# Optimization experiments

Hardware: AMD Instinct MI355X
Metric: run time of the kernel (lower is better)

The kernel has to match this reference:

```python
import jax, jax.numpy as jnp
import numpy as np

IN_FEATURES = 4096
OUT_FEATURES = 4096  # % 16 == 0, so pad_out = 0
BATCH, SEQ = 4, 2048


def setup_inputs() -> dict:
    key = jax.random.key(0)
    k_x, k_w, k_b = jax.random.split(key, 3)
    # int8 activations and weights (W8A8)
    x = jax.random.randint(k_x, (BATCH, SEQ, IN_FEATURES), -128, 128, dtype=jnp.int32).astype(jnp.int8)
    # weight stored as (in_features, out_features), matching qlinear.weight layout
    weight = jax.random.randint(k_w, (IN_FEATURES, OUT_FEATURES), -128, 128, dtype=jnp.int32).astype(jnp.int8)
    # a: scalar input scale; b: per-output-channel dequant/requant scale
    a = jnp.full((1, 1), 0.0123, dtype=jnp.float32)
    b = jax.random.uniform(k_b, (1, OUT_FEATURES), dtype=jnp.float32, minval=0.001, maxval=0.02)
    return {"x": x, "weight": weight, "a": a, "b": b}


def reference(x, weight, a, b):
    # x: [B, S, K] int8; weight: [K, N] int8; a: [1,1] f32; b: [1,N] f32
    x_shape = x.shape
    x2d = x.reshape(-1, x_shape[-1])
    acc = jnp.matmul(x2d, weight, preferred_element_type=jnp.int32)
    # fused dequant (scalar a) + per-channel requant (b), round-to-nearest, saturate to int8
    y_f = acc.astype(jnp.float32) * a * b  # [T, N]
    y = jnp.clip(jnp.round(y_f), -128.0, 127.0).astype(jnp.int8)
    return y.reshape(*x_shape[:-1], -1)
```

## Files before the change

kernel.cpp:

```cpp
#include <hip/hip_runtime.h>
#include <stdint.h>

#define M_DIM 8192
#define N_DIM 4096
#define K_DIM 4096
#define BM 128
#define BN 128
#define BK 64

typedef int v4i __attribute__((ext_vector_type(4)));
typedef unsigned u32;

__device__ __forceinline__ void gll16(const void* g, void* l) {
  __builtin_amdgcn_global_load_lds(
      (const __attribute__((address_space(1))) void*)g,
      (__attribute__((address_space(3))) void*)l, 16, 0, 0);
}

__device__ __forceinline__ u32 pack4(const int4 v) {
  return (v.x & 0xffu) | ((v.y & 0xffu) << 8) | ((v.z & 0xffu) << 16) |
         ((u32)(v.w & 0xffu) << 24);
}

__device__ __forceinline__ bool hdr_is_i32(const int* __restrict__ X, int tid,
                                           int* ok) {
  if (tid == 0) *ok = 1;
  __syncthreads();
  int good = 1;
  for (int i = tid; i < 1024; i += 256) {
    const int w = X[i];
    good &= (w == (int)(int8_t)(w & 0xff));
  }
  if (!good) atomicAnd(ok, 0);
  __syncthreads();
  return *ok != 0;
}

__global__ __launch_bounds__(256) void detect_i32(const int* __restrict__ X,
                                                  u32* __restrict__ flag) {
  __shared__ int ok;
  const bool i32 = hdr_is_i32(X, threadIdx.x, &ok);
  if (threadIdx.x == 0) *flag = i32 ? 1u : 0u;
}

__global__ __launch_bounds__(256) void pack_xw_f(const void* __restrict__ Xin,
                                                 const void* __restrict__ Wv,
                                                 u32* __restrict__ xout,
                                                 int8_t* __restrict__ WT) {
  __shared__ u32 lds[64 * 21];
  __shared__ int ok;
  const int tid = threadIdx.x;
  const bool i32 = hdr_is_i32((const int*)Xin, tid, &ok);

  if (blockIdx.x < 8192) {
    const int base = blockIdx.x * 1024 + tid;
    if (i32) {
      const int4* in = (const int4*)Xin;
#pragma unroll
      for (int j = 0; j < 4; ++j) {
        const int idx = base + j * 256;
        xout[idx] = pack4(in[idx]);
      }
    } else {
      const u32* in = (const u32*)Xin;
#pragma unroll
      for (int j = 0; j < 4; ++j) {
        const int idx = base + j * 256;
        xout[idx] = in[idx];
      }
    }
    return;
  }

  const int bid = blockIdx.x - 8192;
  const int tk = bid & 63;
  const int tn = bid >> 6;
  const int k0 = tk * 64, n0 = tn * 64;

#pragma unroll
  for (int j = 0; j < 4; ++j) {
    const int id = j * 256 + tid;
    const int k = id >> 4, c = id & 15;
    u32 word;
    if (i32) {
      const int4 v =
          *(const int4*)((const int*)Wv + (size_t)(k0 + k) * N_DIM + n0 + c * 4);
      word = pack4(v);
    } else {
      word = *(const u32*)((const int8_t*)Wv + (size_t)(k0 + k) * N_DIM + n0 +
                           c * 4);
    }
    lds[k * 21 + c] = word;
  }
  __syncthreads();
  const int kd = tid & 15, nq = tid >> 4;
  const u32 d0 = lds[(kd * 4 + 0) * 21 + nq];
  const u32 d1 = lds[(kd * 4 + 1) * 21 + nq];
  const u32 d2 = lds[(kd * 4 + 2) * 21 + nq];
  const u32 d3 = lds[(kd * 4 + 3) * 21 + nq];
  u32* outp = (u32*)WT;
#pragma unroll
  for (int i = 0; i < 4; ++i) {
    const u32 e = ((d0 >> (8 * i)) & 0xffu) | (((d1 >> (8 * i)) & 0xffu) << 8) |
                  (((d2 >> (8 * i)) & 0xffu) << 16) |
                  (((d3 >> (8 * i)) & 0xffu) << 24);
    const int n = n0 + nq * 4 + i;
    outp[(size_t)n * (K_DIM / 4) + (k0 / 4) + kd] = e;
  }
}

__global__ __launch_bounds__(256) void packT_w_f(const void* __restrict__ Wv,
                                                 int8_t* __restrict__ WT,
                                                 const int* __restrict__ Xhdr) {
  __shared__ u32 lds[64 * 21];
  __shared__ int ok;
  const int tid = threadIdx.x;
  const bool i32 = hdr_is_i32(Xhdr, tid, &ok);
  const int tk = blockIdx.x & 63;
  const int tn = blockIdx.x >> 6;
  const int k0 = tk * 64, n0 = tn * 64;

#pragma unroll
  for (int j = 0; j < 4; ++j) {
    const int id = j * 256 + tid;
    const int k = id >> 4, c = id & 15;
    u32 word;
    if (i32) {
      const int4 v =
          *(const int4*)((const int*)Wv + (size_t)(k0 + k) * N_DIM + n0 + c * 4);
      word = pack4(v);
    } else {
      word = *(const u32*)((const int8_t*)Wv + (size_t)(k0 + k) * N_DIM + n0 +
                           c * 4);
    }
    lds[k * 21 + c] = word;
  }
  __syncthreads();
  const int kd = tid & 15, nq = tid >> 4;
  const u32 d0 = lds[(kd * 4 + 0) * 21 + nq];
  const u32 d1 = lds[(kd * 4 + 1) * 21 + nq];
  const u32 d2 = lds[(kd * 4 + 2) * 21 + nq];
  const u32 d3 = lds[(kd * 4 + 3) * 21 + nq];
  u32* outp = (u32*)WT;
#pragma unroll
  for (int i = 0; i < 4; ++i) {
    const u32 e = ((d0 >> (8 * i)) & 0xffu) | (((d1 >> (8 * i)) & 0xffu) << 8) |
                  (((d2 >> (8 * i)) & 0xffu) << 16) |
                  (((d3 >> (8 * i)) & 0xffu) << 24);
    const int n = n0 + nq * 4 + i;
    outp[(size_t)n * (K_DIM / 4) + (k0 / 4) + kd] = e;
  }
}

__device__ __forceinline__ void epilogue(const v4i acc[4][4], float a,
                                         const float* __restrict__ bScale,
                                         int* __restrict__ Y, int bm, int bn,
                                         int wm, int wn, int quad, int l16) {
  const int nBase = bn * BN + wn * 64 + l16;
  float bs[4];
#pragma unroll
  for (int ni = 0; ni < 4; ++ni) bs[ni] = bScale[nBase + ni * 16];
#pragma unroll
  for (int mi = 0; mi < 4; ++mi) {
    const int m0 = bm * BM + wm * 64 + mi * 16 + quad * 4;
#pragma unroll
    for (int r = 0; r < 4; ++r) {
      int* row = Y + (size_t)(m0 + r) * N_DIM + nBase;
#pragma unroll
      for (int ni = 0; ni < 4; ++ni) {
        float v = ((float)acc[mi][ni][r] * a) * bs[ni];
        v = rintf(v);
        v = fminf(fmaxf(v, -128.f), 127.f);
        row[ni * 16] = (int)v;
      }
    }
  }
}

__device__ __forceinline__ void rd4(v4i* f, const int8_t* base, int off) {
#pragma unroll
  for (int i = 0; i < 4; ++i) f[i] = *(const v4i*)(base + off + i * 1024);
}

__device__ __forceinline__ void mfma16(v4i acc[8][4], int row, const v4i* a,
                                       const v4i* b) {
#pragma unroll
  for (int mi = 0; mi < 4; ++mi)
#pragma unroll
    for (int ni = 0; ni < 4; ++ni)
      acc[row + mi][ni] = __builtin_amdgcn_mfma_i32_16x16x64_i8(
          a[mi], b[ni], acc[row + mi][ni], 0, 0, 0);
}

__device__ __forceinline__ void compute64(const int8_t* aBase,
                                          const int8_t* bBase, int soff,
                                          v4i acc[8][4]) {
  v4i bf[4], af[4], ag[4];
  rd4(bf, bBase, soff);
  rd4(af, aBase, soff);
  __builtin_amdgcn_s_setprio(1);
  mfma16(acc, 0, af, bf);
  rd4(ag, aBase, soff + 4096);
  mfma16(acc, 4, ag, bf);
  __builtin_amdgcn_s_setprio(0);
}

__global__ __launch_bounds__(512, 2) void gemm_256(
    const int8_t* __restrict__ X, const int8_t* __restrict__ WT,
    const float* __restrict__ aScale, const float* __restrict__ bScale,
    int* __restrict__ Y) {
  __shared__ __align__(16) int8_t lds[131072];
  const int tid = threadIdx.x;
  const int lane = tid & 63;
  const int wave = tid >> 6;
  const int quad = lane >> 4, l16 = lane & 15;
  const int wm = wave >> 2, wn = wave & 3;

  const int swzb = (blockIdx.x & 7) * 64 + (blockIdx.x >> 3);
  const int bn = swzb & 15, bm = swzb >> 4;

  const int clog = (((tid & 3) ^ ((tid >> 3) & 3)) << 4);
  const int pc = quad ^ ((l16 >> 1) & 3);

  const int8_t* xa = X + (size_t)(bm * 256 + (tid >> 2)) * K_DIM + clog;
  const int8_t* xb = WT + (size_t)(bn * 256 + (tid >> 2)) * K_DIM + clog;
  int8_t* ldsA = lds + tid * 16;
  int8_t* ldsB = lds + 65536 + tid * 16;
  const int8_t* aBase = lds + (wm * 128 + l16) * 64 + pc * 16;
  const int8_t* bBase = lds + 65536 + (wn * 64 + l16) * 64 + pc * 16;

  v4i acc[8][4] = {};

#pragma unroll
  for (int t = 0; t < 2; ++t) {
    gll16(xa + t * 64, ldsA + t * 16384);
    gll16(xa + (size_t)128 * K_DIM + t * 64, ldsA + t * 16384 + 8192);
    gll16(xb + t * 64, ldsB + t * 16384);
    gll16(xb + (size_t)128 * K_DIM + t * 64, ldsB + t * 16384 + 8192);
  }
  asm volatile("s_waitcnt vmcnt(0)" ::: "memory");
  __builtin_amdgcn_s_barrier();

  for (int G = 0; G < 32; ++G) {
    const int g0 = 2 * G;
    if (G < 31) {
#pragma unroll
      for (int t = 2; t < 4; ++t) {
        const int poff = ((g0 + t) & 3) << 14;
        const int8_t* sa = xa + (size_t)(g0 + t) * 64;
        const int8_t* sb = xb + (size_t)(g0 + t) * 64;
        gll16(sa, ldsA + poff);
        gll16(sa + (size_t)128 * K_DIM, ldsA + poff + 8192);
        gll16(sb, ldsB + poff);
        gll16(sb + (size_t)128 * K_DIM, ldsB + poff + 8192);
      }
    }
    compute64(aBase, bBase, (g0 & 3) << 14, acc);
    compute64(aBase, bBase, ((g0 + 1) & 3) << 14, acc);
    asm volatile("s_waitcnt vmcnt(0)" ::: "memory");
    __builtin_amdgcn_s_barrier();
  }

  const float a = aScale[0];
  const int nBase = bn * 256 + wn * 64 + l16;
  float bs[4];
#pragma unroll
  for (int ni = 0; ni < 4; ++ni) bs[ni] = bScale[nBase + ni * 16];
#pragma unroll
  for (int mi = 0; mi < 8; ++mi) {
    const int m0 = bm * 256 + wm * 128 + mi * 16 + quad * 4;
#pragma unroll
    for (int r = 0; r < 4; ++r) {
      int* row = Y + (size_t)(m0 + r) * N_DIM + nBase;
#pragma unroll
      for (int ni = 0; ni < 4; ++ni) {
        float v = ((float)acc[mi][ni][r] * a) * bs[ni];
        v = rintf(v);
        v = fminf(fmaxf(v, -128.f), 127.f);
        row[ni * 16] = (int)v;
      }
    }
  }
}

__global__ __launch_bounds__(256) void gemm_inA(
    const void* __restrict__ Xv, const int8_t* __restrict__ WT,
    const float* __restrict__ aScale, const float* __restrict__ bScale,
    int* __restrict__ Y, const u32* __restrict__ flag) {
  __shared__ __align__(16) int8_t As[BM * BK];
  __shared__ __align__(16) int8_t Bs[BN * BK];
  const bool i32 = (*flag != 0);
  const int tid = threadIdx.x;
  const int lane = tid & 63, wave = tid >> 6;
  const int quad = lane >> 4, l16 = lane & 15;
  const int wm = wave & 1, wn = wave >> 1;
  const int bn = blockIdx.x & 31;
  const int bm = blockIdx.x >> 5;

  const int r0 = tid >> 2;
  const int c0 = (tid & 3) * 16;
  const int8_t* Bg0 = WT + (size_t)(bn * BN + r0) * K_DIM + c0;
  const int8_t* Bg1 = Bg0 + (size_t)64 * K_DIM;
  int8_t* Al0 = As + tid * 16;
  int8_t* Al1 = Al0 + 4096;
  int8_t* Bl0 = Bs + tid * 16;
  int8_t* Bl1 = Bl0 + 4096;

  v4i acc[4][4] = {};
  const int8_t* aLds = As + (wm * 64 + l16) * BK + quad * 16;
  const int8_t* bLds = Bs + (wn * 64 + l16) * BK + quad * 16;

  if (i32) {
    const int* Xg0 = (const int*)Xv + (size_t)(bm * BM + r0) * K_DIM + c0;
    const int* Xg1 = Xg0 + (size_t)64 * K_DIM;
    for (int k0 = 0; k0 < K_DIM; k0 += BK) {
      gll16(Bg0 + k0, Bl0);
      gll16(Bg1 + k0, Bl1);
      const int4* p0 = (const int4*)(Xg0 + k0);
      const int4* p1 = (const int4*)(Xg1 + k0);
      uint4 w0, w1;
      w0.x = pack4(p0[0]); w0.y = pack4(p0[1]);
      w0.z = pack4(p0[2]); w0.w = pack4(p0[3]);
      w1.x = pack4(p1[0]); w1.y = pack4(p1[1]);
      w1.z = pack4(p1[2]); w1.w = pack4(p1[3]);
      *(uint4*)Al0 = w0;
      *(uint4*)Al1 = w1;
      __syncthreads();
      v4i af[4], bf[4];
#pragma unroll
      for (int i = 0; i < 4; ++i) af[i] = *(const v4i*)(aLds + i * 16 * BK);
#pragma unroll
      for (int i = 0; i < 4; ++i) bf[i] = *(const v4i*)(bLds + i * 16 * BK);
#pragma unroll
      for (int mi = 0; mi < 4; ++mi)
#pragma unroll
        for (int ni = 0; ni < 4; ++ni)
          acc[mi][ni] = __builtin_amdgcn_mfma_i32_16x16x64_i8(
              af[mi], bf[ni], acc[mi][ni], 0, 0, 0);
      __syncthreads();
    }
  } else {
    const int8_t* Ag0 = (const int8_t*)Xv + (size_t)(bm * BM + r0) * K_DIM + c0;
    const int8_t* Ag1 = Ag0 + (size_t)64 * K_DIM;
    for (int k0 = 0; k0 < K_DIM; k0 += BK) {
      gll16(Ag0 + k0, Al0);
      gll16(Ag1 + k0, Al1);
      gll16(Bg0 + k0, Bl0);
      gll16(Bg1 + k0, Bl1);
      __syncthreads();
      v4i af[4], bf[4];
#pragma unroll
      for (int i = 0; i < 4; ++i) af[i] = *(const v4i*)(aLds + i * 16 * BK);
#pragma unroll
      for (int i = 0; i < 4; ++i) bf[i] = *(const v4i*)(bLds + i * 16 * BK);
#pragma unroll
      for (int mi = 0; mi < 4; ++mi)
#pragma unroll
        for (int ni = 0; ni < 4; ++ni)
          acc[mi][ni] = __builtin_amdgcn_mfma_i32_16x16x64_i8(
              af[mi], bf[ni], acc[mi][ni], 0, 0, 0);
      __syncthreads();
    }
  }
  epilogue(acc, aScale[0], bScale, Y, bm, bn, wm, wn, quad, l16);
}

extern "C" void kernel_launch(void* const* d_in, const int* in_sizes, int n_in,
                              void* d_out, int out_size, void* d_ws,
                              size_t ws_size, hipStream_t stream) {
  const void* Xv = d_in[0];
  const void* Wv = d_in[1];
  const float* a = (const float*)d_in[2];
  const float* b = (const float*)d_in[3];
  int* Y = (int*)d_out;

  const size_t xB = (size_t)M_DIM * K_DIM;
  const size_t wB = (size_t)N_DIM * K_DIM;

  if (ws_size >= xB + wB + 64) {
    int8_t* Xp = (int8_t*)d_ws;
    int8_t* WT = (int8_t*)d_ws + xB;
    pack_xw_f<<<8192 + (K_DIM / 64) * (N_DIM / 64), 256, 0, stream>>>(
        Xv, Wv, (u32*)Xp, WT);
    gemm_256<<<(M_DIM / 256) * (N_DIM / 256), 512, 0, stream>>>(Xp, WT, a, b,
                                                                Y);
  } else if (ws_size >= wB + 64) {
    int8_t* WT = (int8_t*)d_ws;
    u32* flag = (u32*)((int8_t*)d_ws + wB);
    detect_i32<<<1, 256, 0, stream>>>((const int*)Xv, flag);
    packT_w_f<<<(K_DIM / 64) * (N_DIM / 64), 256, 0, stream>>>(Wv, WT,
                                                               (const int*)Xv);
    gemm_inA<<<(M_DIM / BM) * (N_DIM / BN), 256, 0, stream>>>(Xv, WT, a, b, Y,
                                                              flag);
  } else {
    int8_t* WT = (int8_t*)d_ws;
    u32* flag = (u32*)((int8_t*)d_ws + (ws_size >= wB + 4 ? wB : 0));
    detect_i32<<<1, 256, 0, stream>>>((const int*)Xv, flag);
    packT_w_f<<<(K_DIM / 64) * (N_DIM / 64), 256, 0, stream>>>(Wv, WT,
                                                               (const int*)Xv);
    gemm_inA<<<(M_DIM / BM) * (N_DIM / BN), 256, 0, stream>>>(Xv, WT, a, b, Y,
                                                              flag);
  }
}
```

Before: 412.5 us.

## Restructure int8 GEMM main loop into BK=128 double-buffered quarter-phase pipeline

The GEMM now loads 128-wide K tiles with double buffering, splitting each tile into four compute phases. Each phase issues a portion of the next tile's global-to-LDS loads, then runs MFMAs, with barriers and partial vmcnt waits in between. The pack kernels pre-swizzle X and transposed W in global memory (XOR on 16-byte chunks) so that direct LDS loads land in a bank-conflict-free layout matching the new fragment read offsets. This aims to overlap memory traffic with MFMA work more finely and cut LDS bank conflicts, at the cost of many more barriers per iteration and tight coupling between the pack layout and the GEMM indexing.

```diff
diff --git a/kernel.cpp b/kernel.cpp
--- a/kernel.cpp
+++ b/kernel.cpp
@@ -20,6 +20,10 @@
 __device__ __forceinline__ u32 pack4(const int4 v) {
   return (v.x & 0xffu) | ((v.y & 0xffu) << 8) | ((v.z & 0xffu) << 16) |
          ((u32)(v.w & 0xffu) << 24);
+}
+
+__device__ __forceinline__ size_t swz_idx(size_t i) {
+  return i ^ ((((u32)(i >> 10)) & 7u) << 2);
 }
 
 __device__ __forceinline__ bool hdr_is_i32(const int* __restrict__ X, int tid,
@@ -59,14 +63,14 @@
 #pragma unroll
       for (int j = 0; j < 4; ++j) {
         const int idx = base + j * 256;
-        xout[idx] = pack4(in[idx]);
+        xout[swz_idx((size_t)idx)] = pack4(in[idx]);
       }
     } else {
       const u32* in = (const u32*)Xin;
 #pragma unroll
       for (int j = 0; j < 4; ++j) {
         const int idx = base + j * 256;
-        xout[idx] = in[idx];
+        xout[swz_idx((size_t)idx)] = in[idx];
       }
     }
     return;
@@ -105,7 +109,7 @@
                   (((d2 >> (8 * i)) & 0xffu) << 16) |
                   (((d3 >> (8 * i)) & 0xffu) << 24);
     const int n = n0 + nq * 4 + i;
-    outp[(size_t)n * (K_DIM / 4) + (k0 / 4) + kd] = e;
+    outp[swz_idx((size_t)n * (K_DIM / 4) + (k0 / 4) + kd)] = e;
   }
 }
 
@@ -177,11 +181,6 @@
   }
 }
 
-__device__ __forceinline__ void rd4(v4i* f, const int8_t* base, int off) {
-#pragma unroll
-  for (int i = 0; i < 4; ++i) f[i] = *(const v4i*)(base + off + i * 1024);
-}
-
 __device__ __forceinline__ void mfma16(v4i acc[8][4], int row, const v4i* a,
                                        const v4i* b) {
 #pragma unroll
@@ -190,19 +189,6 @@
     for (int ni = 0; ni < 4; ++ni)
       acc[row + mi][ni] = __builtin_amdgcn_mfma_i32_16x16x64_i8(
           a[mi], b[ni], acc[row + mi][ni], 0, 0, 0);
-}
-
-__device__ __forceinline__ void compute64(const int8_t* aBase,
-                                          const int8_t* bBase, int soff,
-                                          v4i acc[8][4]) {
-  v4i bf[4], af[4], ag[4];
-  rd4(bf, bBase, soff);
-  rd4(af, aBase, soff);
-  __builtin_amdgcn_s_setprio(1);
-  mfma16(acc, 0, af, bf);
-  rd4(ag, aBase, soff + 4096);
-  mfma16(acc, 4, ag, bf);
-  __builtin_amdgcn_s_setprio(0);
 }
 
 __global__ __launch_bounds__(512, 2) void gemm_256(
@@ -219,46 +205,113 @@
   const int swzb = (blockIdx.x & 7) * 64 + (blockIdx.x >> 3);
   const int bn = swzb & 15, bm = swzb >> 4;
 
-  const int clog = (((tid & 3) ^ ((tid >> 3) & 3)) << 4);
-  const int pc = quad ^ ((l16 >> 1) & 3);
-
-  const int8_t* xa = X + (size_t)(bm * 256 + (tid >> 2)) * K_DIM + clog;
-  const int8_t* xb = WT + (size_t)(bn * 256 + (tid >> 2)) * K_DIM + clog;
+  const int8_t* xa =
+      X + (size_t)(bm * 256 + (tid >> 3)) * K_DIM + (tid & 7) * 16;
+  const int8_t* xb =
+      WT + (size_t)(bn * 256 + (tid >> 3)) * K_DIM + (tid & 7) * 16;
   int8_t* ldsA = lds + tid * 16;
   int8_t* ldsB = lds + 65536 + tid * 16;
-  const int8_t* aBase = lds + (wm * 128 + l16) * 64 + pc * 16;
-  const int8_t* bBase = lds + 65536 + (wn * 64 + l16) * 64 + pc * 16;
+
+  const int ck0 = ((quad ^ (l16 & 7)) << 4);
+  const int ck1 = (((4 | quad) ^ (l16 & 7)) << 4);
+  const int8_t* aR = lds + l16 * 128;
+  const int8_t* bR = lds + 65536 + l16 * 128;
 
   v4i acc[8][4] = {};
 
-#pragma unroll
-  for (int t = 0; t < 2; ++t) {
-    gll16(xa + t * 64, ldsA + t * 16384);
-    gll16(xa + (size_t)128 * K_DIM + t * 64, ldsA + t * 16384 + 8192);
-    gll16(xb + t * 64, ldsB + t * 16384);
-    gll16(xb + (size_t)128 * K_DIM + t * 64, ldsB + t * 16384 + 8192);
-  }
-  asm volatile("s_waitcnt vmcnt(0)" ::: "memory");
+  gll16(xb + 0 * 262144, ldsB + 0 * 8192);
+  gll16(xb + 1 * 262144, ldsB + 1 * 8192);
+  gll16(xb + 2 * 262144, ldsB + 2 * 8192);
+  gll16(xb + 3 * 262144, ldsB + 3 * 8192);
+  gll16(xa + 0 * 262144, ldsA + 0 * 8192);
+  gll16(xa + 2 * 262144, ldsA + 2 * 8192);
+  gll16(xa + 1 * 262144, ldsA + 1 * 8192);
+  gll16(xa + 3 * 262144, ldsA + 3 * 8192);
+  asm volatile("s_waitcnt vmcnt(2)" ::: "memory");
   __builtin_amdgcn_s_barrier();
 
-  for (int G = 0; G < 32; ++G) {
-    const int g0 = 2 * G;
-    if (G < 31) {
-#pragma unroll
-      for (int t = 2; t < 4; ++t) {
-        const int poff = ((g0 + t) & 3) << 14;
-        const int8_t* sa = xa + (size_t)(g0 + t) * 64;
-        const int8_t* sb = xb + (size_t)(g0 + t) * 64;
-        gll16(sa, ldsA + poff);
-        gll16(sa + (size_t)128 * K_DIM, ldsA + poff + 8192);
-        gll16(sb, ldsB + poff);
-        gll16(sb + (size_t)128 * K_DIM, ldsB + poff + 8192);
-      }
-    }
-    compute64(aBase, bBase, (g0 & 3) << 14, acc);
-    compute64(aBase, bBase, ((g0 + 1) & 3) << 14, acc);
-    asm volatile("s_waitcnt vmcnt(0)" ::: "memory");
-    __builtin_amdgcn_s_barrier();
+  for (int T = 0; T < 32; ++T) {
+    const int sb = (T & 1) * 4;
+    const int sA0 = (sb + wm * 2) * 8192;
+    const int sA1 = (sb + wm * 2 + 1) * 8192;
+    const int sB = (sb + wn) * 8192;
+    const int pB = (sb ^ 4) * 8192;
+    const size_t tOff = (size_t)(T + 1) * 128;
+    const bool st = (T < 31);
+    v4i af[4], bf[4];
+
+#pragma unroll
+    for (int i = 0; i < 4; ++i)
+      af[i] = *(const v4i*)(aR + sA0 + i * 2048 + ck0);
+#pragma unroll
+    for (int n = 0; n < 4; ++n)
+      bf[n] = *(const v4i*)(bR + sB + n * 2048 + ck0);
+    if (st) {
+      gll16(xb + tOff, ldsB + pB);
+      gll16(xb + 262144 + tOff, ldsB + pB + 8192);
+    }
+    __builtin_amdgcn_s_barrier();
+    asm volatile("s_waitcnt lgkmcnt(0)" ::: "memory");
+    __builtin_amdgcn_sched_barrier(0);
+    __builtin_amdgcn_s_setprio(1);
+    mfma16(acc, 0, af, bf);
+    __builtin_amdgcn_s_setprio(0);
+    if (st)
+      asm volatile("s_waitcnt vmcnt(2)" ::: "memory");
+    else
+      asm volatile("s_waitcnt vmcnt(0)" ::: "memory");
+    __builtin_amdgcn_s_barrier();
+
+#pragma unroll
+    for (int i = 0; i < 4; ++i)
+      af[i] = *(const v4i*)(aR + sA1 + i * 2048 + ck0);
+    if (st) {
+      gll16(xb + 2 * 262144 + tOff, ldsB + pB + 2 * 8192);
+      gll16(xb + 3 * 262144 + tOff, ldsB + pB + 3 * 8192);
+    }
+    __builtin_amdgcn_s_barrier();
+    asm volatile("s_waitcnt lgkmcnt(0)" ::: "memory");
+    __builtin_amdgcn_sched_barrier(0);
+    __builtin_amdgcn_s_setprio(1);
+    mfma16(acc, 4, af, bf);
+    __builtin_amdgcn_s_setprio(0);
+    __builtin_amdgcn_s_barrier();
+
+#pragma unroll
+    for (int i = 0; i < 4; ++i)
+      af[i] = *(const v4i*)(aR + sA0 + i * 2048 + ck1);
+#pragma unroll
+    for (int n = 0; n < 4; ++n)
+      bf[n] = *(const v4i*)(bR + sB + n * 2048 + ck1);
+    if (st) {
+      gll16(xa + tOff, ldsA + pB);
+      gll16(xa + 2 * 262144 + tOff, ldsA + pB + 2 * 8192);
+    }
+    __builtin_amdgcn_s_barrier();
+    asm volatile("s_waitcnt lgkmcnt(0)" ::: "memory");
+    __builtin_amdgcn_sched_barrier(0);
+    __builtin_amdgcn_s_setprio(1);
+    mfma16(acc, 0, af, bf);
+    __builtin_amdgcn_s_setprio(0);
+    __builtin_amdgcn_s_barrier();
+
+#pragma unroll
+    for (int i = 0; i < 4; ++i)
+      af[i] = *(const v4i*)(aR + sA1 + i * 2048 + ck1);
+    if (st) {
+      gll16(xa + 262144 + tOff, ldsA + pB + 8192);
+      gll16(xa + 3 * 262144 + tOff, ldsA + pB + 3 * 8192);
+    }
+    __builtin_amdgcn_s_barrier();
+    asm volatile("s_waitcnt lgkmcnt(0)" ::: "memory");
+    __builtin_amdgcn_sched_barrier(0);
+    __builtin_amdgcn_s_setprio(1);
+    mfma16(acc, 4, af, bf);
+    __builtin_amdgcn_s_setprio(0);
+    if (st) {
+      asm volatile("s_waitcnt vmcnt(2)" ::: "memory");
+      __builtin_amdgcn_s_barrier();
+    }
   }
 
   const float a = aScale[0];
```

After: 389.4 us. -5.6%, faster.
